# Kernel optimization log

Hardware: AMD Instinct MI355X
Metric: run time of the kernel (lower is better)

The kernel has to match this reference:

```python
import jax, jax.numpy as jnp
import numpy as np

B, N, C, H = 2, 2048, 1024, 16
D = C // H
SCALE = D ** -0.5


def setup_inputs() -> dict:
    key = jax.random.key(0)
    ks = jax.random.split(key, 4)
    s = 0.02
    return {
        "x": jax.random.normal(ks[0], (B, N, C), dtype=jnp.float32),
        "f": jax.random.normal(ks[1], (B, N, C), dtype=jnp.float32),
        "W_qkv": jax.random.normal(ks[2], (C, 3 * C), dtype=jnp.float32) * s,
        "W_proj": jax.random.normal(ks[3], (C, C), dtype=jnp.float32) * s,
        "b_proj": jnp.zeros((C,), dtype=jnp.float32),
    }


def reference(x, f, W_qkv, W_proj, b_proj):
    b, n, c = x.shape
    h, d = H, c // H
    # qkv projection -> (B,N,3,H,D) -> q,k,v each (B,H,N,D)
    qkv = (x @ W_qkv).reshape(b, n, 3, h, d)
    q = jnp.transpose(qkv[:, :, 0], (0, 2, 1, 3))
    k = jnp.transpose(qkv[:, :, 1], (0, 2, 1, 3))
    v = jnp.transpose(qkv[:, :, 2], (0, 2, 1, 3))
    # full NxN scores, faithful to the original manual MHA
    attn = jax.nn.softmax(jnp.einsum("bhqd,bhkd->bhqk", q, k) * SCALE, axis=-1)
    av = jnp.einsum("bhqk,bhkd->bhqd", attn, v)  # (B,H,N,D)
    # pre-residual output branch
    attn2gcn = jnp.transpose(av, (0, 2, 1, 3)).reshape(b, n, c)
    # residual fuse with f (reshaped per-head in torch; equivalent to flat add)
    fused = attn2gcn + f
    out = fused @ W_proj + b_proj
    return (out, attn2gcn)
```

## Files before the change

kernel.cpp:

```cpp
#include <hip/hip_runtime.h>
#include <hip/hip_bf16.h>

#define OUT1_OFF 4194304
#define QSCALE 0.1803368801111204f

typedef __attribute__((ext_vector_type(8))) short bf16x8;
typedef __attribute__((ext_vector_type(4))) float f32x4;

__device__ __forceinline__ unsigned short f2bf(float x) {
    unsigned u = __float_as_uint(x);
    u += 0x7FFFu + ((u >> 16) & 1u);
    return (unsigned short)(u >> 16);
}

__device__ __forceinline__ void gl2lds16(const unsigned short* g, unsigned short* l) {
    __builtin_amdgcn_global_load_lds(
        (const __attribute__((address_space(1))) unsigned int*)g,
        (__attribute__((address_space(3))) unsigned int*)l, 16, 0, 0);
}

__global__ __launch_bounds__(256) void prep(const float* __restrict__ x,
                                            const float* __restrict__ Wqkv,
                                            const float* __restrict__ Wproj,
                                            unsigned short* __restrict__ xb,
                                            unsigned short* __restrict__ wqkvT,
                                            unsigned short* __restrict__ wprojT) {
    __shared__ float T[64][65];
    const int bid = blockIdx.x, tid = threadIdx.x;
    if (bid < 4096) {
        int i = bid * 256 + tid;
        float4 v = reinterpret_cast<const float4*>(x)[i];
        ushort4 o = make_ushort4(f2bf(v.x), f2bf(v.y), f2bf(v.z), f2bf(v.w));
        reinterpret_cast<ushort4*>(xb)[i] = o;
        return;
    }
    const float* in; unsigned short* out; int Nd, bx, by;
    if (bid < 4864) { int t = bid - 4096; in = Wqkv;  out = wqkvT;  Nd = 3072; bx = t % 48; by = t / 48; }
    else            { int t = bid - 4864; in = Wproj; out = wprojT; Nd = 1024; bx = t % 16; by = t / 16; }
    const int Kd = 1024;
    const int r0 = by * 64, c0 = bx * 64;
    const int tr = tid >> 3, tc = (tid & 7) * 8;
#pragma unroll
    for (int rr = 0; rr < 64; rr += 32) {
        const float4* p = reinterpret_cast<const float4*>(&in[(r0 + tr + rr) * Nd + c0 + tc]);
        float4 v0 = p[0], v1 = p[1];
        T[tr + rr][tc + 0] = v0.x; T[tr + rr][tc + 1] = v0.y;
        T[tr + rr][tc + 2] = v0.z; T[tr + rr][tc + 3] = v0.w;
        T[tr + rr][tc + 4] = v1.x; T[tr + rr][tc + 5] = v1.y;
        T[tr + rr][tc + 6] = v1.z; T[tr + rr][tc + 7] = v1.w;
    }
    __syncthreads();
#pragma unroll
    for (int rr = 0; rr < 64; rr += 32) {
        int orow = tr + rr;
        ushort4 o0 = make_ushort4(f2bf(T[tc + 0][orow]), f2bf(T[tc + 1][orow]),
                                  f2bf(T[tc + 2][orow]), f2bf(T[tc + 3][orow]));
        ushort4 o1 = make_ushort4(f2bf(T[tc + 4][orow]), f2bf(T[tc + 5][orow]),
                                  f2bf(T[tc + 6][orow]), f2bf(T[tc + 7][orow]));
        unsigned short* dst = &out[(c0 + orow) * Kd + r0 + tc];
        *reinterpret_cast<ushort4*>(dst) = o0;
        *reinterpret_cast<ushort4*>(dst + 4) = o1;
    }
}

__global__ __launch_bounds__(256) void gemm_qkv(const unsigned short* __restrict__ A,
                                                const unsigned short* __restrict__ Bt,
                                                unsigned short* __restrict__ qb,
                                                unsigned short* __restrict__ kb,
                                                unsigned short* __restrict__ vtb) {
    __shared__ __align__(16) unsigned short Sh[16384];
    unsigned short* As = Sh;
    unsigned short* Bs = Sh + 8192;
    const int tid = threadIdx.x;
    const int w = tid >> 6, lane = tid & 63, quad = lane >> 4, l15 = lane & 15;
    const int m0 = blockIdx.y * 128, n0 = blockIdx.x * 128;
    const int wm = (w & 1) * 64, wn = (w >> 1) * 64;
    const int sw = (l15 & 7) << 3;
    f32x4 acc[4][4] = {};
    for (int k0 = 0; k0 < 1024; k0 += 64) {
        __syncthreads();
#pragma unroll
        for (int t = 0; t < 4; ++t) {
            int c = t * 256 + tid;
            int row = c >> 3, jg = ((c & 7) ^ (row & 7)) * 8;
            gl2lds16(&A[(m0 + row) * 1024 + k0 + jg], &As[c * 8]);
            gl2lds16(&Bt[(n0 + row) * 1024 + k0 + jg], &Bs[c * 8]);
        }
        __syncthreads();
#pragma unroll
        for (int kk = 0; kk < 2; ++kk) {
            bf16x8 af[4], bfr[4];
#pragma unroll
            for (int i = 0; i < 4; ++i)
                af[i] = *reinterpret_cast<const bf16x8*>(
                    &As[(wm + i * 16 + l15) * 64 + ((((kk * 4 + quad) << 3) ^ sw))]);
#pragma unroll
            for (int j = 0; j < 4; ++j)
                bfr[j] = *reinterpret_cast<const bf16x8*>(
                    &Bs[(wn + j * 16 + l15) * 64 + ((((kk * 4 + quad) << 3) ^ sw))]);
#pragma unroll
            for (int i = 0; i < 4; ++i)
#pragma unroll
                for (int j = 0; j < 4; ++j)
                    acc[i][j] = __builtin_amdgcn_mfma_f32_16x16x32_bf16(af[i], bfr[j], acc[i][j], 0, 0, 0);
        }
    }
    const int nbase = n0 + wn;
    const int t = nbase >> 10;
    __syncthreads();
    if (t < 2) {
#pragma unroll
        for (int j = 0; j < 4; ++j) {
            int n = nbase + j * 16 + l15;
            int h = (n & 1023) >> 6, dd = n & 63;
#pragma unroll
            for (int i = 0; i < 4; ++i)
#pragma unroll
                for (int r = 0; r < 4; ++r) {
                    int m = m0 + wm + i * 16 + quad * 4 + r;
                    int b = m >> 11, tok = m & 2047;
                    float v = acc[i][j][r];
                    if (t == 0) qb[(((b * 16 + h) * 2048) + tok) * 64 + dd] = f2bf(v * QSCALE);
                    else        kb[(((b * 16 + h) * 2048) + tok) * 64 + dd] = f2bf(v);
                }
        }
    } else {
        unsigned short* scr = Sh + w * 4096;
        const int mb = m0 + wm;
        const int b = mb >> 11, kblk = (mb & 2047) >> 6;
        const int h = (nbase & 1023) >> 6;
#pragma unroll
        for (int i = 0; i < 4; ++i) {
            int slot0 = ((i & 2) << 4) | (quad << 3) | ((i & 1) << 2);
#pragma unroll
            for (int j = 0; j < 4; ++j) {
                unsigned short h0 = f2bf(acc[i][j][0]), h1 = f2bf(acc[i][j][1]);
                unsigned short h2 = f2bf(acc[i][j][2]), h3 = f2bf(acc[i][j][3]);
                uint2 pk = make_uint2((unsigned)h0 | ((unsigned)h1 << 16),
                                      (unsigned)h2 | ((unsigned)h3 << 16));
                *reinterpret_cast<uint2*>(&scr[(j * 16 + l15) * 64 + slot0]) = pk;
            }
        }
        asm volatile("s_waitcnt lgkmcnt(0)" ::: "memory");
        unsigned short* vtile = vtb + (((b * 16 + h) * 32) + kblk) * 4096;
#pragma unroll
        for (int p = 0; p < 8; ++p) {
            int idx = (p * 64 + lane) * 8;
            *reinterpret_cast<uint4*>(&vtile[idx]) = *reinterpret_cast<const uint4*>(&scr[idx]);
        }
    }
}

__global__ __launch_bounds__(256) void attn_kernel(const unsigned short* __restrict__ qb,
                                                   const unsigned short* __restrict__ kb,
                                                   const unsigned short* __restrict__ vtb,
                                                   const float* __restrict__ f,
                                                   float* __restrict__ attn2_out,
                                                   unsigned short* __restrict__ fusedb) {
    __shared__ __align__(16) unsigned short Ksw[2][4096];
    __shared__ __align__(16) unsigned short Vsw[2][4096];
    const int tid = threadIdx.x;
    const int w = tid >> 6, lane = tid & 63, quad = lane >> 4, l15 = lane & 15;
    const int bh = blockIdx.x;
    const int q0 = blockIdx.y * 64 + w * 16;
    const unsigned short* qr = &qb[(bh * 2048 + q0 + l15) * 64 + quad * 8];
    bf16x8 ql0 = *reinterpret_cast<const bf16x8*>(qr);
    bf16x8 ql1 = *reinterpret_cast<const bf16x8*>(qr + 32);
    const unsigned short* kt0 = kb + bh * 131072;
    const unsigned short* vt0 = vtb + bh * 131072;
    const int c1 = tid, c2 = tid + 256;
    const int gu1 = (((c1 & ~7) | ((c1 & 7) ^ ((c1 >> 3) & 7))) << 3);
    const int gu2 = (((c2 & ~7) | ((c2 & 7) ^ ((c2 >> 3) & 7))) << 3);
    const int sw = (l15 & 7) << 3;
    f32x4 O[4] = {};
    f32x4 asum = {};
    bf16x8 ones;
#pragma unroll
    for (int j = 0; j < 8; ++j) ones[j] = (short)0x3F80;

#define STAGE(IT, BUF) do { int _toff = (IT) * 4096;                    \
        gl2lds16(kt0 + _toff + gu1, &Ksw[BUF][c1 * 8]);                 \
        gl2lds16(kt0 + _toff + gu2, &Ksw[BUF][c2 * 8]);                 \
        gl2lds16(vt0 + _toff + gu1, &Vsw[BUF][c1 * 8]);                 \
        gl2lds16(vt0 + _toff + gu2, &Vsw[BUF][c2 * 8]); } while (0)

    auto body = [&](int buf) {
        f32x4 T[4];
#pragma unroll
        for (int s = 0; s < 4; ++s) {
            const unsigned short* kr = &Ksw[buf][(s * 16 + l15) * 64];
            bf16x8 k0 = *reinterpret_cast<const bf16x8*>(&kr[(quad << 3) ^ sw]);
            bf16x8 k1 = *reinterpret_cast<const bf16x8*>(&kr[((quad + 4) << 3) ^ sw]);
            f32x4 z = {};
            z = __builtin_amdgcn_mfma_f32_16x16x32_bf16(k0, ql0, z, 0, 0, 0);
            z = __builtin_amdgcn_mfma_f32_16x16x32_bf16(k1, ql1, z, 0, 0, 0);
            T[s] = z;
        }
        float p[4][4];
#pragma unroll
        for (int s = 0; s < 4; ++s)
#pragma unroll
            for (int r = 0; r < 4; ++r) p[s][r] = __builtin_amdgcn_exp2f(T[s][r]);
        uint4 u0, u1;
        u0.x = __builtin_amdgcn_perm(__float_as_uint(p[0][1]), __float_as_uint(p[0][0]), 0x07060302u);
        u0.y = __builtin_amdgcn_perm(__float_as_uint(p[0][3]), __float_as_uint(p[0][2]), 0x07060302u);
        u0.z = __builtin_amdgcn_perm(__float_as_uint(p[1][1]), __float_as_uint(p[1][0]), 0x07060302u);
        u0.w = __builtin_amdgcn_perm(__float_as_uint(p[1][3]), __float_as_uint(p[1][2]), 0x07060302u);
        u1.x = __builtin_amdgcn_perm(__float_as_uint(p[2][1]), __float_as_uint(p[2][0]), 0x07060302u);
        u1.y = __builtin_amdgcn_perm(__float_as_uint(p[2][3]), __float_as_uint(p[2][2]), 0x07060302u);
        u1.z = __builtin_amdgcn_perm(__float_as_uint(p[3][1]), __float_as_uint(p[3][0]), 0x07060302u);
        u1.w = __builtin_amdgcn_perm(__float_as_uint(p[3][3]), __float_as_uint(p[3][2]), 0x07060302u);
        bf16x8 pa0 = __builtin_bit_cast(bf16x8, u0);
        bf16x8 pa1 = __builtin_bit_cast(bf16x8, u1);
        asum = __builtin_amdgcn_mfma_f32_16x16x32_bf16(pa0, ones, asum, 0, 0, 0);
        asum = __builtin_amdgcn_mfma_f32_16x16x32_bf16(pa1, ones, asum, 0, 0, 0);
#pragma unroll
        for (int c4 = 0; c4 < 4; ++c4) {
            const unsigned short* vr = &Vsw[buf][(c4 * 16 + l15) * 64];
            bf16x8 v0 = *reinterpret_cast<const bf16x8*>(&vr[(quad << 3) ^ sw]);
            bf16x8 v1 = *reinterpret_cast<const bf16x8*>(&vr[((quad + 4) << 3) ^ sw]);
            O[c4] = __builtin_amdgcn_mfma_f32_16x16x32_bf16(pa0, v0, O[c4], 0, 0, 0);
            O[c4] = __builtin_amdgcn_mfma_f32_16x16x32_bf16(pa1, v1, O[c4], 0, 0, 0);
        }
    };

    STAGE(0, 0);
    for (int it = 0; it < 32; it += 2) {
        __syncthreads();
        STAGE(it + 1, 1);
        body(0);
        __syncthreads();
        if (it + 2 < 32) STAGE(it + 2, 0);
        body(1);
    }
#undef STAGE

    const int b = bh >> 4, h = bh & 15;
#pragma unroll
    for (int r = 0; r < 4; ++r) {
        float inv = 1.f / asum[r];
        int tok = q0 + quad * 4 + r;
        int base = (b * 2048 + tok) * 1024 + h * 64;
#pragma unroll
        for (int c4 = 0; c4 < 4; ++c4) {
            int col = c4 * 16 + l15;
            float o = O[c4][r] * inv;
            attn2_out[base + col] = o;
            fusedb[base + col] = f2bf(o + f[base + col]);
        }
    }
}

__global__ __launch_bounds__(256) void gemm_proj(const unsigned short* __restrict__ A,
                                                 const unsigned short* __restrict__ Bt,
                                                 const float* __restrict__ bias,
                                                 float* __restrict__ out) {
    __shared__ __align__(16) unsigned short As[4096];
    __shared__ __align__(16) unsigned short Bs[4096];
    const int tid = threadIdx.x;
    const int w = tid >> 6, lane = tid & 63, quad = lane >> 4, l15 = lane & 15;
    const int m0 = blockIdx.y * 64, n0 = blockIdx.x * 64;
    const int wm = (w & 1) * 32, wn = (w >> 1) * 32;
    const int sw = (l15 & 7) << 3;
    f32x4 acc[2][2] = {};
    for (int k0 = 0; k0 < 1024; k0 += 64) {
        __syncthreads();
#pragma unroll
        for (int t = 0; t < 2; ++t) {
            int c = t * 256 + tid;
            int row = c >> 3, jg = ((c & 7) ^ (row & 7)) * 8;
            gl2lds16(&A[(m0 + row) * 1024 + k0 + jg], &As[c * 8]);
            gl2lds16(&Bt[(n0 + row) * 1024 + k0 + jg], &Bs[c * 8]);
        }
        __syncthreads();
#pragma unroll
        for (int kk = 0; kk < 2; ++kk) {
            bf16x8 af[2], bfr[2];
#pragma unroll
            for (int i = 0; i < 2; ++i)
                af[i] = *reinterpret_cast<const bf16x8*>(
                    &As[(wm + i * 16 + l15) * 64 + ((((kk * 4 + quad) << 3) ^ sw))]);
#pragma unroll
            for (int j = 0; j < 2; ++j)
                bfr[j] = *reinterpret_cast<const bf16x8*>(
                    &Bs[(wn + j * 16 + l15) * 64 + ((((kk * 4 + quad) << 3) ^ sw))]);
#pragma unroll
            for (int i = 0; i < 2; ++i)
#pragma unroll
                for (int j = 0; j < 2; ++j)
                    acc[i][j] = __builtin_amdgcn_mfma_f32_16x16x32_bf16(af[i], bfr[j], acc[i][j], 0, 0, 0);
        }
    }
#pragma unroll
    for (int j = 0; j < 2; ++j) {
        int n = n0 + wn + j * 16 + l15;
        float bv = bias[n];
#pragma unroll
        for (int i = 0; i < 2; ++i)
#pragma unroll
            for (int r = 0; r < 4; ++r) {
                int m = m0 + wm + i * 16 + quad * 4 + r;
                out[m * 1024 + n] = acc[i][j][r] + bv;
            }
    }
}

extern "C" void kernel_launch(void* const* d_in, const int* in_sizes, int n_in,
                              void* d_out, int out_size, void* d_ws, size_t ws_size,
                              hipStream_t stream) {
    const float* x      = (const float*)d_in[0];
    const float* f      = (const float*)d_in[1];
    const float* W_qkv  = (const float*)d_in[2];
    const float* W_proj = (const float*)d_in[3];
    const float* b_proj = (const float*)d_in[4];
    float* out   = (float*)d_out;
    float* attn2 = out + OUT1_OFF;

    char* ws = (char*)d_ws;
    unsigned short* xb     = (unsigned short*)(ws);
    unsigned short* wqkvT  = (unsigned short*)(ws + 8388608);
    unsigned short* wprojT = (unsigned short*)(ws + 14680064);
    unsigned short* qb     = (unsigned short*)(ws + 16777216);
    unsigned short* kb     = (unsigned short*)(ws + 25165824);
    unsigned short* vtb    = (unsigned short*)(ws + 33554432);
    unsigned short* fusedb = (unsigned short*)(ws + 41943040);

    prep<<<5120, 256, 0, stream>>>(x, W_qkv, W_proj, xb, wqkvT, wprojT);
    gemm_qkv<<<dim3(24, 32), 256, 0, stream>>>(xb, wqkvT, qb, kb, vtb);
    attn_kernel<<<dim3(32, 32), 256, 0, stream>>>(qb, kb, vtb, f, attn2, fusedb);
    gemm_proj<<<dim3(16, 64), 256, 0, stream>>>(fusedb, wprojT, b_proj, out);
}
```

Baseline: 199.9 us.

## Stage Q/K epilogue through LDS, widen attention blocks, enlarge proj tiles

The QKV GEMM swaps MFMA operands for Q/K tiles and stages results through padded LDS scratch. This gives coalesced 16-byte stores to the q/k buffers instead of scattered 2-byte stores. The attention kernel moves to 512-thread blocks covering 128 queries, so each block's K/V tile loads are shared across twice as many waves. The projection GEMM grows its M tile to 128 for more reuse per B load, at the cost of fewer blocks and higher register and LDS use.

```diff
diff --git a/kernel.cpp b/kernel.cpp
--- a/kernel.cpp
+++ b/kernel.cpp
@@ -68,20 +68,23 @@
                                                 unsigned short* __restrict__ qb,
                                                 unsigned short* __restrict__ kb,
                                                 unsigned short* __restrict__ vtb) {
-    __shared__ __align__(16) unsigned short Sh[16384];
+    __shared__ __align__(16) unsigned short Sh[18432];
     unsigned short* As = Sh;
     unsigned short* Bs = Sh + 8192;
     const int tid = threadIdx.x;
     const int w = tid >> 6, lane = tid & 63, quad = lane >> 4, l15 = lane & 15;
     const int m0 = blockIdx.y * 128, n0 = blockIdx.x * 128;
     const int wm = (w & 1) * 64, wn = (w >> 1) * 64;
+    const int nbase = n0 + wn;
+    const int t = nbase >> 10;
+    const bool qk = (t < 2);
     const int sw = (l15 & 7) << 3;
     f32x4 acc[4][4] = {};
     for (int k0 = 0; k0 < 1024; k0 += 64) {
         __syncthreads();
 #pragma unroll
-        for (int t = 0; t < 4; ++t) {
-            int c = t * 256 + tid;
+        for (int tt = 0; tt < 4; ++tt) {
+            int c = tt * 256 + tid;
             int row = c >> 3, jg = ((c & 7) ^ (row & 7)) * 8;
             gl2lds16(&A[(m0 + row) * 1024 + k0 + jg], &As[c * 8]);
             gl2lds16(&Bt[(n0 + row) * 1024 + k0 + jg], &Bs[c * 8]);
@@ -98,37 +101,50 @@
             for (int j = 0; j < 4; ++j)
                 bfr[j] = *reinterpret_cast<const bf16x8*>(
                     &Bs[(wn + j * 16 + l15) * 64 + ((((kk * 4 + quad) << 3) ^ sw))]);
-#pragma unroll
-            for (int i = 0; i < 4; ++i)
-#pragma unroll
-                for (int j = 0; j < 4; ++j)
-                    acc[i][j] = __builtin_amdgcn_mfma_f32_16x16x32_bf16(af[i], bfr[j], acc[i][j], 0, 0, 0);
-        }
-    }
-    const int nbase = n0 + wn;
-    const int t = nbase >> 10;
+            if (qk) {
+#pragma unroll
+                for (int i = 0; i < 4; ++i)
+#pragma unroll
+                    for (int j = 0; j < 4; ++j)
+                        acc[i][j] = __builtin_amdgcn_mfma_f32_16x16x32_bf16(bfr[j], af[i], acc[i][j], 0, 0, 0);
+            } else {
+#pragma unroll
+                for (int i = 0; i < 4; ++i)
+#pragma unroll
+                    for (int j = 0; j < 4; ++j)
+                        acc[i][j] = __builtin_amdgcn_mfma_f32_16x16x32_bf16(af[i], bfr[j], acc[i][j], 0, 0, 0);
+            }
+        }
+    }
     __syncthreads();
-    if (t < 2) {
-#pragma unroll
-        for (int j = 0; j < 4; ++j) {
-            int n = nbase + j * 16 + l15;
-            int h = (n & 1023) >> 6, dd = n & 63;
-#pragma unroll
-            for (int i = 0; i < 4; ++i)
-#pragma unroll
-                for (int r = 0; r < 4; ++r) {
-                    int m = m0 + wm + i * 16 + quad * 4 + r;
-                    int b = m >> 11, tok = m & 2047;
-                    float v = acc[i][j][r];
-                    if (t == 0) qb[(((b * 16 + h) * 2048) + tok) * 64 + dd] = f2bf(v * QSCALE);
-                    else        kb[(((b * 16 + h) * 2048) + tok) * 64 + dd] = f2bf(v);
-                }
+    unsigned short* scr = Sh + w * 4608;
+    const int mb = m0 + wm;
+    const int b = mb >> 11;
+    const int h = (nbase & 1023) >> 6;
+    const float sc = (t == 0) ? QSCALE : 1.f;
+    if (qk) {
+#pragma unroll
+        for (int i = 0; i < 4; ++i) {
+            int row = i * 16 + l15;
+#pragma unroll
+            for (int j = 0; j < 4; ++j) {
+                unsigned short h0 = f2bf(acc[i][j][0] * sc), h1 = f2bf(acc[i][j][1] * sc);
+                unsigned short h2 = f2bf(acc[i][j][2] * sc), h3 = f2bf(acc[i][j][3] * sc);
+                uint2 pk = make_uint2((unsigned)h0 | ((unsigned)h1 << 16),
+                                      (unsigned)h2 | ((unsigned)h3 << 16));
+                *reinterpret_cast<uint2*>(&scr[row * 72 + j * 16 + quad * 4]) = pk;
+            }
+        }
+        asm volatile("s_waitcnt lgkmcnt(0)" ::: "memory");
+        unsigned short* dst = (t == 0 ? qb : kb) + (((b * 16 + h) * 2048) + (mb & 2047)) * 64;
+#pragma unroll
+        for (int p = 0; p < 8; ++p) {
+            int idx = p * 64 + lane;
+            *reinterpret_cast<uint4*>(&dst[idx * 8]) =
+                *reinterpret_cast<const uint4*>(&scr[(idx >> 3) * 72 + (idx & 7) * 8]);
         }
     } else {
-        unsigned short* scr = Sh + w * 4096;
-        const int mb = m0 + wm;
-        const int b = mb >> 11, kblk = (mb & 2047) >> 6;
-        const int h = (nbase & 1023) >> 6;
+        const int kblk = (mb & 2047) >> 6;
 #pragma unroll
         for (int i = 0; i < 4; ++i) {
             int slot0 = ((i & 2) << 4) | (quad << 3) | ((i & 1) << 2);
@@ -138,20 +154,21 @@
                 unsigned short h2 = f2bf(acc[i][j][2]), h3 = f2bf(acc[i][j][3]);
                 uint2 pk = make_uint2((unsigned)h0 | ((unsigned)h1 << 16),
                                       (unsigned)h2 | ((unsigned)h3 << 16));
-                *reinterpret_cast<uint2*>(&scr[(j * 16 + l15) * 64 + slot0]) = pk;
+                *reinterpret_cast<uint2*>(&scr[(j * 16 + l15) * 72 + slot0]) = pk;
             }
         }
         asm volatile("s_waitcnt lgkmcnt(0)" ::: "memory");
         unsigned short* vtile = vtb + (((b * 16 + h) * 32) + kblk) * 4096;
 #pragma unroll
         for (int p = 0; p < 8; ++p) {
-            int idx = (p * 64 + lane) * 8;
-            *reinterpret_cast<uint4*>(&vtile[idx]) = *reinterpret_cast<const uint4*>(&scr[idx]);
-        }
-    }
-}
-
-__global__ __launch_bounds__(256) void attn_kernel(const unsigned short* __restrict__ qb,
+            int idx = p * 64 + lane;
+            *reinterpret_cast<uint4*>(&vtile[idx * 8]) =
+                *reinterpret_cast<const uint4*>(&scr[(idx >> 3) * 72 + (idx & 7) * 8]);
+        }
+    }
+}
+
+__global__ __launch_bounds__(512) void attn_kernel(const unsigned short* __restrict__ qb,
                                                    const unsigned short* __restrict__ kb,
                                                    const unsigned short* __restrict__ vtb,
                                                    const float* __restrict__ f,
@@ -162,15 +179,14 @@
     const int tid = threadIdx.x;
     const int w = tid >> 6, lane = tid & 63, quad = lane >> 4, l15 = lane & 15;
     const int bh = blockIdx.x;
-    const int q0 = blockIdx.y * 64 + w * 16;
+    const int q0 = blockIdx.y * 128 + w * 16;
     const unsigned short* qr = &qb[(bh * 2048 + q0 + l15) * 64 + quad * 8];
     bf16x8 ql0 = *reinterpret_cast<const bf16x8*>(qr);
     bf16x8 ql1 = *reinterpret_cast<const bf16x8*>(qr + 32);
     const unsigned short* kt0 = kb + bh * 131072;
     const unsigned short* vt0 = vtb + bh * 131072;
-    const int c1 = tid, c2 = tid + 256;
-    const int gu1 = (((c1 & ~7) | ((c1 & 7) ^ ((c1 >> 3) & 7))) << 3);
-    const int gu2 = (((c2 & ~7) | ((c2 & 7) ^ ((c2 >> 3) & 7))) << 3);
+    const int c = tid;
+    const int gu = (((c & ~7) | ((c & 7) ^ ((c >> 3) & 7))) << 3);
     const int sw = (l15 & 7) << 3;
     f32x4 O[4] = {};
     f32x4 asum = {};
@@ -179,10 +195,8 @@
     for (int j = 0; j < 8; ++j) ones[j] = (short)0x3F80;
 
 #define STAGE(IT, BUF) do { int _toff = (IT) * 4096;                    \
-        gl2lds16(kt0 + _toff + gu1, &Ksw[BUF][c1 * 8]);                 \
-        gl2lds16(kt0 + _toff + gu2, &Ksw[BUF][c2 * 8]);                 \
-        gl2lds16(vt0 + _toff + gu1, &Vsw[BUF][c1 * 8]);                 \
-        gl2lds16(vt0 + _toff + gu2, &Vsw[BUF][c2 * 8]); } while (0)
+        gl2lds16(kt0 + _toff + gu, &Ksw[BUF][c * 8]);                   \
+        gl2lds16(vt0 + _toff + gu, &Vsw[BUF][c * 8]); } while (0)
 
     auto body = [&](int buf) {
         f32x4 T[4];
@@ -255,29 +269,29 @@
                                                  const unsigned short* __restrict__ Bt,
                                                  const float* __restrict__ bias,
                                                  float* __restrict__ out) {
-    __shared__ __align__(16) unsigned short As[4096];
+    __shared__ __align__(16) unsigned short As[8192];
     __shared__ __align__(16) unsigned short Bs[4096];
     const int tid = threadIdx.x;
     const int w = tid >> 6, lane = tid & 63, quad = lane >> 4, l15 = lane & 15;
-    const int m0 = blockIdx.y * 64, n0 = blockIdx.x * 64;
-    const int wm = (w & 1) * 32, wn = (w >> 1) * 32;
+    const int m0 = blockIdx.y * 128, n0 = blockIdx.x * 64;
+    const int wm = (w & 1) * 64, wn = (w >> 1) * 32;
     const int sw = (l15 & 7) << 3;
-    f32x4 acc[2][2] = {};
+    f32x4 acc[4][2] = {};
     for (int k0 = 0; k0 < 1024; k0 += 64) {
         __syncthreads();
 #pragma unroll
-        for (int t = 0; t < 2; ++t) {
+        for (int t = 0; t < 4; ++t) {
             int c = t * 256 + tid;
             int row = c >> 3, jg = ((c & 7) ^ (row & 7)) * 8;
             gl2lds16(&A[(m0 + row) * 1024 + k0 + jg], &As[c * 8]);
-            gl2lds16(&Bt[(n0 + row) * 1024 + k0 + jg], &Bs[c * 8]);
+            if (t < 2) gl2lds16(&Bt[(n0 + row) * 1024 + k0 + jg], &Bs[c * 8]);
         }
         __syncthreads();
 #pragma unroll
         for (int kk = 0; kk < 2; ++kk) {
-            bf16x8 af[2], bfr[2];
-#pragma unroll
-            for (int i = 0; i < 2; ++i)
+            bf16x8 af[4], bfr[2];
+#pragma unroll
+            for (int i = 0; i < 4; ++i)
                 af[i] = *reinterpret_cast<const bf16x8*>(
                     &As[(wm + i * 16 + l15) * 64 + ((((kk * 4 + quad) << 3) ^ sw))]);
 #pragma unroll
@@ -285,7 +299,7 @@
                 bfr[j] = *reinterpret_cast<const bf16x8*>(
                     &Bs[(wn + j * 16 + l15) * 64 + ((((kk * 4 + quad) << 3) ^ sw))]);
 #pragma unroll
-            for (int i = 0; i < 2; ++i)
+            for (int i = 0; i < 4; ++i)
 #pragma unroll
                 for (int j = 0; j < 2; ++j)
                     acc[i][j] = __builtin_amdgcn_mfma_f32_16x16x32_bf16(af[i], bfr[j], acc[i][j], 0, 0, 0);
@@ -296,7 +310,7 @@
         int n = n0 + wn + j * 16 + l15;
         float bv = bias[n];
 #pragma unroll
-        for (int i = 0; i < 2; ++i)
+        for (int i = 0; i < 4; ++i)
 #pragma unroll
             for (int r = 0; r < 4; ++r) {
                 int m = m0 + wm + i * 16 + quad * 4 + r;
@@ -327,6 +341,6 @@
 
     prep<<<5120, 256, 0, stream>>>(x, W_qkv, W_proj, xb, wqkvT, wprojT);
     gemm_qkv<<<dim3(24, 32), 256, 0, stream>>>(xb, wqkvT, qb, kb, vtb);
-    attn_kernel<<<dim3(32, 32), 256, 0, stream>>>(qb, kb, vtb, f, attn2, fusedb);
-    gemm_proj<<<dim3(16, 64), 256, 0, stream>>>(fusedb, wprojT, b_proj, out);
-}
+    attn_kernel<<<dim3(32, 16), 512, 0, stream>>>(qb, kb, vtb, f, attn2, fusedb);
+    gemm_proj<<<dim3(16, 32), 256, 0, stream>>>(fusedb, wprojT, b_proj, out);
+}
```

Result: faster. 189.1 us (-5.4%).
